# Kernel optimization log

Hardware: AMD Instinct MI355X
Metric: run time of the kernel (lower is better)

## Reference

```python
import jax, jax.numpy as jnp
import numpy as np

DIMS = [30, 64, 32, 16, 8, 2]

def _kaiming_uniform(key, fan_out, fan_in):
    # torch kaiming_uniform_ default: a=0 -> gain=sqrt(2), bound=gain*sqrt(3/fan_in)
    bound = np.sqrt(2.0) * np.sqrt(3.0 / fan_in)
    return jax.random.uniform(key, (fan_out, fan_in), jnp.float32, -bound, bound)

def setup_inputs() -> dict:
    key = jax.random.key(0)
    ks = jax.random.split(key, 6)
    inp = {"x": jax.random.normal(ks[0], (1000000, DIMS[0]), jnp.float32)}
    for i in range(5):
        inp[f"w{i+1}"] = _kaiming_uniform(ks[i + 1], DIMS[i + 1], DIMS[i])
        inp[f"b{i+1}"] = jnp.zeros((DIMS[i + 1],), jnp.float32)
    return inp

def reference(x, w1, b1, w2, b2, w3, b3, w4, b4, w5, b5):
    # quant/dequant stubs are identity in fp32 mode
    h = jax.nn.relu(x @ w1.T + b1)
    h = jax.nn.relu(h @ w2.T + b2)
    h = jax.nn.relu(h @ w3.T + b3)
    h = jax.nn.relu(h @ w4.T + b4)
    return h @ w5.T + b5
```

## Files before the change

kernel.cpp:

```cpp
#include <hip/hip_runtime.h>


typedef float        f32x4 __attribute__((ext_vector_type(4)));
typedef unsigned int u32x4 __attribute__((ext_vector_type(4)));
typedef short        s16x8 __attribute__((ext_vector_type(8)));

static __device__ __forceinline__ unsigned short f2bf(float f) {
    return __builtin_bit_cast(unsigned short, (__bf16)f);
}
static __device__ __forceinline__ unsigned int pkbf(float a, float b) {
    return (unsigned int)f2bf(a) | ((unsigned int)f2bf(b) << 16);
}
static __device__ __forceinline__ unsigned int rp2(float a, float b) {
    return pkbf(fmaxf(a, 0.0f), fmaxf(b, 0.0f));
}

#define MFMA(A, B, C) __builtin_amdgcn_mfma_f32_16x16x32_bf16((A), (B), (C), 0, 0, 0)

#define OW1 0
#define OW2 1920
#define OW3 3968
#define OW4 4480
#define OW5 4608
#define OB1 4624
#define OB2 4688
#define OB3 4720
#define OB4 4736
#define OB5 4744
#define WTOT 4746

__global__ __launch_bounds__(256) void mlp_mfma_kernel(
    const float* __restrict__ x,
    const float* __restrict__ w1, const float* __restrict__ b1,
    const float* __restrict__ w2, const float* __restrict__ b2,
    const float* __restrict__ w3, const float* __restrict__ b3,
    const float* __restrict__ w4, const float* __restrict__ b4,
    const float* __restrict__ w5, const float* __restrict__ b5,
    float* __restrict__ out, int n)
{
    __shared__ float W[WTOT];

    const int tid  = threadIdx.x;
    const int lane = tid & 63;
    const int wv   = tid >> 6;
    const int g    = lane >> 4;
    const int ml   = lane & 15;

    for (int i = tid; i < 1920; i += 256) W[OW1 + i] = w1[i];
    for (int i = tid; i < 2048; i += 256) W[OW2 + i] = w2[i];
    for (int i = tid; i < 512;  i += 256) W[OW3 + i] = w3[i];
    if (tid < 128) W[OW4 + tid] = w4[tid];
    if (tid < 16)  W[OW5 + tid] = w5[tid];
    if (tid < 64)  W[OB1 + tid] = b1[tid];
    if (tid < 32)  W[OB2 + tid] = b2[tid];
    if (tid < 16)  W[OB3 + tid] = b3[tid];
    if (tid < 8)   W[OB4 + tid] = b4[tid];
    if (tid < 2)   W[OB5 + tid] = b5[tid];
    __syncthreads();

    s16x8 A1[4], A2[2][2], A3, A4, A5;
    #pragma unroll
    for (int t = 0; t < 4; ++t) {
        #pragma unroll
        for (int i = 0; i < 8; ++i) {
            const int k = 4*g + (i & 3) + ((i >> 2) << 4);
            const int m = 16*t + ml;
            float v = (k < 30) ? W[OW1 + m*30 + k] : ((k == 30) ? W[OB1 + m] : 0.0f);
            A1[t][i] = (short)f2bf(v);
        }
    }
    #pragma unroll
    for (int t = 0; t < 2; ++t)
        #pragma unroll
        for (int s = 0; s < 2; ++s)
            #pragma unroll
            for (int i = 0; i < 8; ++i) {
                const int k = 4*g + (i & 3) + ((i >> 2) << 4);
                A2[t][s][i] = (short)f2bf(W[OW2 + (16*t + ml)*64 + 32*s + k]);
            }
    #pragma unroll
    for (int i = 0; i < 8; ++i) {
        const int k = 4*g + (i & 3) + ((i >> 2) << 4);
        A3[i] = (short)f2bf(W[OW3 + ml*32 + k]);
        float v4 = 0.0f, v5 = 0.0f;
        if (ml < 8) v4 = (k < 16) ? W[OW4 + ml*16 + k] : ((k == 16) ? W[OB4 + ml] : 0.0f);
        if (ml < 2) v5 = (k <  8) ? W[OW5 + ml*8  + k] : ((k ==  8) ? W[OB5 + ml] : 0.0f);
        A4[i] = (short)f2bf(v4);
        A5[i] = (short)f2bf(v5);
    }
    f32x4 bias2[2], bias3;
    #pragma unroll
    for (int t = 0; t < 2; ++t)
        #pragma unroll
        for (int q = 0; q < 4; ++q)
            bias2[t][q] = W[OB2 + 16*t + 4*g + q];
    #pragma unroll
    for (int q = 0; q < 4; ++q)
        bias3[q] = W[OB3 + 4*g + q];

    const int ntiles = (n + 15) >> 4;
    const int npairs = (ntiles + 1) >> 1;
    const int NW = gridDim.x * 4;
    int p = blockIdx.x * 4 + wv;
    if (p >= npairs) return;

    auto loadx = [&](int t, f32x4& xa, f32x4& xb) {
        int row = t*16 + ml;
        if (row >= n) row = n - 1;
        const float* rp = x + (size_t)row * 30;
        float2 a01 = *(const float2*)(rp + 4*g);
        float2 a23 = *(const float2*)(rp + 4*g + 2);
        xa[0] = a01.x; xa[1] = a01.y; xa[2] = a23.x; xa[3] = a23.y;
        if (g < 3) {
            float2 b01 = *(const float2*)(rp + 16 + 4*g);
            float2 b23 = *(const float2*)(rp + 18 + 4*g);
            xb[0] = b01.x; xb[1] = b01.y; xb[2] = b23.x; xb[3] = b23.y;
        } else {
            float2 b01 = *(const float2*)(rp + 28);
            xb[0] = b01.x; xb[1] = b01.y;
            xb[2] = 1.0f;
            xb[3] = 0.0f;
        }
    };

    f32x4 xa[2], xb[2];
    {
        const int t0 = 2*p;
        loadx(t0, xa[0], xb[0]);
        int t1 = t0 + 1; if (t1 >= ntiles) t1 = ntiles - 1;
        loadx(t1, xa[1], xb[1]);
    }

    const f32x4 zero = {0.0f, 0.0f, 0.0f, 0.0f};

    while (true) {
        const int np_ = p + NW;
        const bool have_next = (np_ < npairs);
        f32x4 nxa[2], nxb[2];
        if (have_next) {
            const int t0 = 2*np_;
            loadx(t0, nxa[0], nxb[0]);
            int t1 = t0 + 1; if (t1 >= ntiles) t1 = ntiles - 1;
            loadx(t1, nxa[1], nxb[1]);
        }

        s16x8 B0[2];
        #pragma unroll
        for (int j = 0; j < 2; ++j) {
            u32x4 u0;
            u0.x = pkbf(xa[j][0], xa[j][1]); u0.y = pkbf(xa[j][2], xa[j][3]);
            u0.z = pkbf(xb[j][0], xb[j][1]); u0.w = pkbf(xb[j][2], xb[j][3]);
            B0[j] = __builtin_bit_cast(s16x8, u0);
        }
        f32x4 c1[2][4];
        #pragma unroll
        for (int t = 0; t < 4; ++t)
            #pragma unroll
            for (int j = 0; j < 2; ++j)
                c1[j][t] = MFMA(A1[t], B0[j], zero);

        s16x8 B1[2][2];
        #pragma unroll
        for (int j = 0; j < 2; ++j)
            #pragma unroll
            for (int s = 0; s < 2; ++s) {
                u32x4 u;
                u.x = rp2(c1[j][2*s][0],     c1[j][2*s][1]);
                u.y = rp2(c1[j][2*s][2],     c1[j][2*s][3]);
                u.z = rp2(c1[j][2*s + 1][0], c1[j][2*s + 1][1]);
                u.w = rp2(c1[j][2*s + 1][2], c1[j][2*s + 1][3]);
                B1[j][s] = __builtin_bit_cast(s16x8, u);
            }
        f32x4 c2[2][2];
        #pragma unroll
        for (int t = 0; t < 2; ++t)
            #pragma unroll
            for (int j = 0; j < 2; ++j) {
                f32x4 a = bias2[t];
                #pragma unroll
                for (int s = 0; s < 2; ++s) a = MFMA(A2[t][s], B1[j][s], a);
                c2[j][t] = a;
            }

        f32x4 c3[2];
        #pragma unroll
        for (int j = 0; j < 2; ++j) {
            u32x4 u2;
            u2.x = rp2(c2[j][0][0], c2[j][0][1]);
            u2.y = rp2(c2[j][0][2], c2[j][0][3]);
            u2.z = rp2(c2[j][1][0], c2[j][1][1]);
            u2.w = rp2(c2[j][1][2], c2[j][1][3]);
            c3[j] = MFMA(A3, __builtin_bit_cast(s16x8, u2), bias3);
        }

        f32x4 c4[2];
        #pragma unroll
        for (int j = 0; j < 2; ++j) {
            u32x4 u3;
            u3.x = rp2(c3[j][0], c3[j][1]);
            u3.y = rp2(c3[j][2], c3[j][3]);
            u3.z = (g == 0) ? 0x3F80u : 0u;
            u3.w = 0u;
            c4[j] = MFMA(A4, __builtin_bit_cast(s16x8, u3), zero);
        }

        f32x4 c5[2];
        #pragma unroll
        for (int j = 0; j < 2; ++j) {
            u32x4 u4;
            u4.x = (g == 2) ? 0x3F80u : rp2(c4[j][0], c4[j][1]);
            u4.y = (g == 2) ? 0u      : rp2(c4[j][2], c4[j][3]);
            u4.z = 0u; u4.w = 0u;
            c5[j] = MFMA(A5, __builtin_bit_cast(s16x8, u4), zero);
        }

        #pragma unroll
        for (int j = 0; j < 2; ++j) {
            const int tj = 2*p + j;
            const int orow = tj*16 + lane;
            if (tj < ntiles && lane < 16 && orow < n) {
                float2 o; o.x = c5[j][0]; o.y = c5[j][1];
                *(float2*)(out + (size_t)orow * 2) = o;
            }
        }

        if (!have_next) break;
        #pragma unroll
        for (int j = 0; j < 2; ++j) { xa[j] = nxa[j]; xb[j] = nxb[j]; }
        p = np_;
    }
}

extern "C" void kernel_launch(void* const* d_in, const int* in_sizes, int n_in,
                              void* d_out, int out_size, void* d_ws, size_t ws_size,
                              hipStream_t stream) {
    const float* x  = (const float*)d_in[0];
    const float* w1 = (const float*)d_in[1];
    const float* b1 = (const float*)d_in[2];
    const float* w2 = (const float*)d_in[3];
    const float* b2 = (const float*)d_in[4];
    const float* w3 = (const float*)d_in[5];
    const float* b3 = (const float*)d_in[6];
    const float* w4 = (const float*)d_in[7];
    const float* b4 = (const float*)d_in[8];
    const float* w5 = (const float*)d_in[9];
    const float* b5 = (const float*)d_in[10];
    float* out = (float*)d_out;

    const int n = in_sizes[0] / 30;
    const int ntiles = (n + 15) >> 4;
    const int npairs = (ntiles + 1) >> 1;
    int blocks = (npairs + 3) / 4;
    if (blocks > 2048) blocks = 2048;

    mlp_mfma_kernel<<<blocks, 256, 0, stream>>>(
        x, w1, b1, w2, b2, w3, b3, w4, b4, w5, b5, out, n);
}
```

Measured before the change: 49.30 us.

## Stream input tiles into LDS via async global_load_lds triple buffering

Replaces per-lane strided register loads of x with contiguous 16-byte and 4-byte global_load_lds transfers into a per-wave three-slot LDS ring, prefetching two pairs ahead and controlled by explicit vmcnt waits. Weights are now read straight from global memory instead of being staged through a shared buffer with a block barrier. Bias1 is folded into the MFMA accumulator rather than into an augmented input column. The grid is capped at fewer blocks so each wave runs a longer persistent loop. This aims for coalesced, deeper-pipelined streaming of the dominant input read, at the cost of relying on hand-written waitcnt counts and a separate tail path.

```diff
diff --git a/kernel.cpp b/kernel.cpp
--- a/kernel.cpp
+++ b/kernel.cpp
@@ -15,19 +15,21 @@
     return pkbf(fmaxf(a, 0.0f), fmaxf(b, 0.0f));
 }
 
+static __device__ __forceinline__ void gld16(const void* g, void* l) {
+    __builtin_amdgcn_global_load_lds(
+        (const __attribute__((address_space(1))) unsigned int*)g,
+        (__attribute__((address_space(3))) unsigned int*)l, 16, 0, 0);
+}
+static __device__ __forceinline__ void gld4(const void* g, void* l) {
+    __builtin_amdgcn_global_load_lds(
+        (const __attribute__((address_space(1))) unsigned int*)g,
+        (__attribute__((address_space(3))) unsigned int*)l, 4, 0, 0);
+}
+
 #define MFMA(A, B, C) __builtin_amdgcn_mfma_f32_16x16x32_bf16((A), (B), (C), 0, 0, 0)
 
-#define OW1 0
-#define OW2 1920
-#define OW3 3968
-#define OW4 4480
-#define OW5 4608
-#define OB1 4624
-#define OB2 4688
-#define OB3 4720
-#define OB4 4736
-#define OB5 4744
-#define WTOT 4746
+#define SLOT_B 4096
+#define NSLOT  3
 
 __global__ __launch_bounds__(256) void mlp_mfma_kernel(
     const float* __restrict__ x,
@@ -38,25 +40,18 @@
     const float* __restrict__ w5, const float* __restrict__ b5,
     float* __restrict__ out, int n)
 {
-    __shared__ float W[WTOT];
-
-    const int tid  = threadIdx.x;
-    const int lane = tid & 63;
-    const int wv   = tid >> 6;
+    __shared__ __attribute__((aligned(16))) unsigned char ldsX[4][NSLOT * SLOT_B];
+
+    const int lane = threadIdx.x & 63;
+    const int wv   = threadIdx.x >> 6;
     const int g    = lane >> 4;
     const int ml   = lane & 15;
 
-    for (int i = tid; i < 1920; i += 256) W[OW1 + i] = w1[i];
-    for (int i = tid; i < 2048; i += 256) W[OW2 + i] = w2[i];
-    for (int i = tid; i < 512;  i += 256) W[OW3 + i] = w3[i];
-    if (tid < 128) W[OW4 + tid] = w4[tid];
-    if (tid < 16)  W[OW5 + tid] = w5[tid];
-    if (tid < 64)  W[OB1 + tid] = b1[tid];
-    if (tid < 32)  W[OB2 + tid] = b2[tid];
-    if (tid < 16)  W[OB3 + tid] = b3[tid];
-    if (tid < 8)   W[OB4 + tid] = b4[tid];
-    if (tid < 2)   W[OB5 + tid] = b5[tid];
-    __syncthreads();
+    unsigned char* myL = &ldsX[wv][0];
+
+    #pragma unroll
+    for (int s = 0; s < NSLOT; ++s)
+        *(unsigned int*)(myL + s * SLOT_B + 3840 + lane * 4) = 0u;
 
     s16x8 A1[4], A2[2][2], A3, A4, A5;
     #pragma unroll
@@ -65,7 +60,7 @@
         for (int i = 0; i < 8; ++i) {
             const int k = 4*g + (i & 3) + ((i >> 2) << 4);
             const int m = 16*t + ml;
-            float v = (k < 30) ? W[OW1 + m*30 + k] : ((k == 30) ? W[OB1 + m] : 0.0f);
+            float v = (k < 30) ? w1[m*30 + k] : 0.0f;
             A1[t][i] = (short)f2bf(v);
         }
     }
@@ -76,88 +71,111 @@
             #pragma unroll
             for (int i = 0; i < 8; ++i) {
                 const int k = 4*g + (i & 3) + ((i >> 2) << 4);
-                A2[t][s][i] = (short)f2bf(W[OW2 + (16*t + ml)*64 + 32*s + k]);
+                A2[t][s][i] = (short)f2bf(w2[(16*t + ml)*64 + 32*s + k]);
             }
     #pragma unroll
     for (int i = 0; i < 8; ++i) {
         const int k = 4*g + (i & 3) + ((i >> 2) << 4);
-        A3[i] = (short)f2bf(W[OW3 + ml*32 + k]);
+        A3[i] = (short)f2bf(w3[ml*32 + k]);
         float v4 = 0.0f, v5 = 0.0f;
-        if (ml < 8) v4 = (k < 16) ? W[OW4 + ml*16 + k] : ((k == 16) ? W[OB4 + ml] : 0.0f);
-        if (ml < 2) v5 = (k <  8) ? W[OW5 + ml*8  + k] : ((k ==  8) ? W[OB5 + ml] : 0.0f);
+        if (ml < 8) v4 = (k < 16) ? w4[ml*16 + k] : ((k == 16) ? b4[ml] : 0.0f);
+        if (ml < 2) v5 = (k <  8) ? w5[ml*8  + k] : ((k ==  8) ? b5[ml] : 0.0f);
         A4[i] = (short)f2bf(v4);
         A5[i] = (short)f2bf(v5);
     }
-    f32x4 bias2[2], bias3;
+    f32x4 bias1[4], bias2[2], bias3;
+    #pragma unroll
+    for (int t = 0; t < 4; ++t)
+        #pragma unroll
+        for (int q = 0; q < 4; ++q)
+            bias1[t][q] = b1[16*t + 4*g + q];
     #pragma unroll
     for (int t = 0; t < 2; ++t)
         #pragma unroll
         for (int q = 0; q < 4; ++q)
-            bias2[t][q] = W[OB2 + 16*t + 4*g + q];
+            bias2[t][q] = b2[16*t + 4*g + q];
     #pragma unroll
     for (int q = 0; q < 4; ++q)
-        bias3[q] = W[OB3 + 4*g + q];
+        bias3[q] = b3[4*g + q];
 
     const int ntiles = (n + 15) >> 4;
     const int npairs = (ntiles + 1) >> 1;
     const int NW = gridDim.x * 4;
-    int p = blockIdx.x * 4 + wv;
-    if (p >= npairs) return;
-
-    auto loadx = [&](int t, f32x4& xa, f32x4& xb) {
-        int row = t*16 + ml;
-        if (row >= n) row = n - 1;
-        const float* rp = x + (size_t)row * 30;
-        float2 a01 = *(const float2*)(rp + 4*g);
-        float2 a23 = *(const float2*)(rp + 4*g + 2);
-        xa[0] = a01.x; xa[1] = a01.y; xa[2] = a23.x; xa[3] = a23.y;
-        if (g < 3) {
-            float2 b01 = *(const float2*)(rp + 16 + 4*g);
-            float2 b23 = *(const float2*)(rp + 18 + 4*g);
-            xb[0] = b01.x; xb[1] = b01.y; xb[2] = b23.x; xb[3] = b23.y;
+    const int p0 = blockIdx.x * 4 + wv;
+    if (p0 >= npairs) return;
+
+    const size_t xbytes = (size_t)n * 120;
+
+    auto issue = [&](int pr, int sl) {
+        size_t gb = (size_t)pr * 3840;
+        if (gb + 3840 > xbytes) gb = xbytes - 3840;
+        const unsigned char* gp = (const unsigned char*)x + gb;
+        unsigned char* lp = myL + sl * SLOT_B;
+        gld16(gp +        (size_t)lane * 16, lp);
+        gld16(gp + 1024 + (size_t)lane * 16, lp + 1024);
+        gld16(gp + 2048 + (size_t)lane * 16, lp + 2048);
+        gld4 (gp + 3072 + (size_t)lane * 4,  lp + 3072);
+        gld4 (gp + 3328 + (size_t)lane * 4,  lp + 3328);
+        gld4 (gp + 3584 + (size_t)lane * 4,  lp + 3584);
+    };
+
+    issue(p0, 0);
+    if (p0 + NW < npairs) issue(p0 + NW, 1);
+
+    const f32x4 zero = {0.0f, 0.0f, 0.0f, 0.0f};
+    int slot = 0;
+
+    for (int p = p0; p < npairs; p += NW) {
+        const int pf = p + 2 * NW;
+        if (pf < npairs) {
+            int s2 = slot + 2; if (s2 >= NSLOT) s2 -= NSLOT;
+            issue(pf, s2);
+            asm volatile("s_waitcnt vmcnt(12)" ::: "memory");
+        } else if (p + NW < npairs) {
+            asm volatile("s_waitcnt vmcnt(6)" ::: "memory");
         } else {
-            float2 b01 = *(const float2*)(rp + 28);
-            xb[0] = b01.x; xb[1] = b01.y;
-            xb[2] = 1.0f;
-            xb[3] = 0.0f;
-        }
-    };
-
-    f32x4 xa[2], xb[2];
-    {
-        const int t0 = 2*p;
-        loadx(t0, xa[0], xb[0]);
-        int t1 = t0 + 1; if (t1 >= ntiles) t1 = ntiles - 1;
-        loadx(t1, xa[1], xb[1]);
-    }
-
-    const f32x4 zero = {0.0f, 0.0f, 0.0f, 0.0f};
-
-    while (true) {
-        const int np_ = p + NW;
-        const bool have_next = (np_ < npairs);
-        f32x4 nxa[2], nxb[2];
-        if (have_next) {
-            const int t0 = 2*np_;
-            loadx(t0, nxa[0], nxb[0]);
-            int t1 = t0 + 1; if (t1 >= ntiles) t1 = ntiles - 1;
-            loadx(t1, nxa[1], nxb[1]);
+            asm volatile("s_waitcnt vmcnt(0)" ::: "memory");
         }
 
         s16x8 B0[2];
-        #pragma unroll
-        for (int j = 0; j < 2; ++j) {
-            u32x4 u0;
-            u0.x = pkbf(xa[j][0], xa[j][1]); u0.y = pkbf(xa[j][2], xa[j][3]);
-            u0.z = pkbf(xb[j][0], xb[j][1]); u0.w = pkbf(xb[j][2], xb[j][3]);
-            B0[j] = __builtin_bit_cast(s16x8, u0);
-        }
+        const bool fullpair = ((p + 1) * 32 <= n);
+        if (fullpair) {
+            const float* L = (const float*)(myL + slot * SLOT_B);
+            #pragma unroll
+            for (int j = 0; j < 2; ++j) {
+                const float* rp = L + (16*j + ml) * 30 + 4*g;
+                float2 a01 = *(const float2*)(rp);
+                float2 a23 = *(const float2*)(rp + 2);
+                float2 b01 = *(const float2*)(rp + 16);
+                float2 b23 = *(const float2*)(rp + 18);
+                u32x4 u;
+                u.x = pkbf(a01.x, a01.y); u.y = pkbf(a23.x, a23.y);
+                u.z = pkbf(b01.x, b01.y); u.w = pkbf(b23.x, b23.y);
+                B0[j] = __builtin_bit_cast(s16x8, u);
+            }
+        } else {
+            #pragma unroll
+            for (int j = 0; j < 2; ++j) {
+                int row = p*32 + 16*j + ml;
+                if (row >= n) row = n - 1;
+                const float* rp = x + (size_t)row * 30 + 4*g;
+                float2 a01 = *(const float2*)(rp);
+                float2 a23 = *(const float2*)(rp + 2);
+                float2 b01 = *(const float2*)(rp + 16);
+                float2 b23 = (g < 3) ? *(const float2*)(rp + 18) : make_float2(0.f, 0.f);
+                u32x4 u;
+                u.x = pkbf(a01.x, a01.y); u.y = pkbf(a23.x, a23.y);
+                u.z = pkbf(b01.x, b01.y); u.w = pkbf(b23.x, b23.y);
+                B0[j] = __builtin_bit_cast(s16x8, u);
+            }
+        }
+
         f32x4 c1[2][4];
         #pragma unroll
         for (int t = 0; t < 4; ++t)
             #pragma unroll
             for (int j = 0; j < 2; ++j)
-                c1[j][t] = MFMA(A1[t], B0[j], zero);
+                c1[j][t] = MFMA(A1[t], B0[j], bias1[t]);
 
         s16x8 B1[2][2];
         #pragma unroll
@@ -216,18 +234,14 @@
 
         #pragma unroll
         for (int j = 0; j < 2; ++j) {
-            const int tj = 2*p + j;
-            const int orow = tj*16 + lane;
-            if (tj < ntiles && lane < 16 && orow < n) {
+            const int orow = (2*p + j)*16 + lane;
+            if (lane < 16 && orow < n) {
                 float2 o; o.x = c5[j][0]; o.y = c5[j][1];
                 *(float2*)(out + (size_t)orow * 2) = o;
             }
         }
 
-        if (!have_next) break;
-        #pragma unroll
-        for (int j = 0; j < 2; ++j) { xa[j] = nxa[j]; xb[j] = nxb[j]; }
-        p = np_;
+        slot = (slot + 1 == NSLOT) ? 0 : slot + 1;
     }
 }
 
@@ -251,7 +265,7 @@
     const int ntiles = (n + 15) >> 4;
     const int npairs = (ntiles + 1) >> 1;
     int blocks = (npairs + 3) / 4;
-    if (blocks > 2048) blocks = 2048;
+    if (blocks > 768) blocks = 768;
 
     mlp_mfma_kernel<<<blocks, 256, 0, stream>>>(
         x, w1, b1, w2, b2, w3, b3, w4, b4, w5, b5, out, n);
```

Measured after the change: 44.58 us. 9.6% less time.
